# Kernel optimization log

Hardware: AMD Instinct MI355X
Metric: run time of the kernel (lower is better)

The kernel has to match this reference:

```python
import jax, jax.numpy as jnp
import numpy as np

N = 1024          # num_features
H = N // 2        # core dimension (num_params // 2)
NB = 4            # num_blocks
B = 16384         # batch


def _lifted_core(rot_params, diag_params):
    """Build the (N, N) lifted core matrix for one Cayley block."""
    # skew-symmetric matrix from the H rotation params
    S = rot_params[:, None] - rot_params[None, :]            # (H, H)
    I = jnp.eye(H, dtype=rot_params.dtype)
    rotation = jnp.linalg.solve(I - S, I + S)                # Cayley transform
    core = diag_params[:, None] * rotation                   # diag(d) @ rotation
    # rot90(core, k=o) only depends on o mod 4 -> precompute 4 variants
    rots = jnp.stack([core,
                      jnp.rot90(core, 1),
                      jnp.rot90(core, 2),
                      jnp.rot90(core, 3)])                   # (4, H, H)

    def body(lifted, o):
        blk = jax.lax.dynamic_slice(lifted, (o, o), (H, H)) + rots[o % 4]
        return jax.lax.dynamic_update_slice(lifted, blk, (o, o)), None

    lifted, _ = jax.lax.scan(body, jnp.zeros((N, N), dtype=core.dtype),
                             jnp.arange(H + 1))
    return lifted


def setup_inputs() -> dict:
    key = jax.random.key(0)
    ks = jax.random.split(key, 5)
    x = jax.random.normal(ks[0], (B, N), dtype=jnp.float32)
    enc_rot = jax.random.normal(ks[1], (NB, H), dtype=jnp.float32)
    enc_diag = jax.random.normal(ks[2], (NB, H), dtype=jnp.float32)
    dec_rot = jax.random.normal(ks[3], (NB, H), dtype=jnp.float32)
    dec_diag = jax.random.normal(ks[4], (NB, H), dtype=jnp.float32)
    return {"x": x, "enc_rot": enc_rot, "enc_diag": enc_diag,
            "dec_rot": dec_rot, "dec_diag": dec_diag}


def reference(x, enc_rot, enc_diag, dec_rot, dec_diag):
    s = x
    for i in range(NB):                                      # encoder blocks
        s = s @ _lifted_core(enc_rot[i], enc_diag[i]).T
    bottleneck = s
    out = s
    for i in range(NB):                                      # decoder blocks
        out = out @ _lifted_core(dec_rot[i], dec_diag[i]).T
    return bottleneck, out
```

## Files before the change

### kernel.cpp

```cpp
#include <hip/hip_runtime.h>
#include <hip/hip_bf16.h>
#include <cstdint>
#include <cstddef>

#define H 512
#define NFEAT 1024
#define BATCH 16384
#define LM ((size_t)1 << 20)
#define KOP 576

using bf16 = __hip_bfloat16;
using bf16x8 = __attribute__((ext_vector_type(8))) __bf16;
using f32x4 = __attribute__((ext_vector_type(4))) float;
using f32x16 = __attribute__((ext_vector_type(16))) float;

__device__ __forceinline__ void gload16(void* lds, const void* g) {
  __builtin_amdgcn_global_load_lds(
      (__attribute__((address_space(1))) void*)g,
      (__attribute__((address_space(3))) void*)lds,
      16, 0, 0);
}

__global__ void prep_kernel(const float* __restrict__ er, const float* __restrict__ ed,
                            const float* __restrict__ dr, const float* __restrict__ dd,
                            float* __restrict__ ab) {
  const int mat = blockIdx.x;
  const int lane = threadIdx.x;
  const float* u = (mat < 4) ? (er + mat * H) : (dr + (mat - 4) * H);
  const float* d = (mat < 4) ? (ed + mat * H) : (dd + (mat - 4) * H);

  double s = 0.0, q = 0.0;
  for (int k = 0; k < 8; ++k) {
    double v = (double)u[lane + 64 * k];
    s += v;
    q += v * v;
  }
  for (int off = 32; off; off >>= 1) {
    s += __shfl_down(s, off);
    q += __shfl_down(q, off);
  }
  s = __shfl(s, 0);
  q = __shfl(q, 0);

  const double det = 1.0 - s * s + (double)H * q;
  const double cuv = 2.0 * (1.0 + s) / det;
  const double cuu = -2.0 * (double)H / det;
  const double cvv = -2.0 * q / det;
  const double cvu = -2.0 * (1.0 - s) / det;

  float* a = ab + mat * 1024;
  float* b = a + H;
  for (int k = 0; k < 8; ++k) {
    int idx = lane + 64 * k;
    double ui = (double)u[idx], di = (double)d[idx];
    a[idx] = (float)(di * (cuv * ui + cvv));
    b[idx] = (float)(di * (cuu * ui + cvu));
  }
}

__global__ __launch_bounds__(256) void prep2_kernel(
    const float* __restrict__ er, const float* __restrict__ ed,
    const float* __restrict__ dr, const float* __restrict__ dd,
    const float* __restrict__ ab, float* __restrict__ Tpref) {
  __shared__ float buf[4][512];
  __shared__ float tmp[4][512];
  const int mat = blockIdx.x;
  const float* d = (mat < 4) ? (ed + mat * H) : (dd + (mat - 4) * H);
  const float* a = ab + mat * 1024;
  const int t = threadIdx.x;
  for (int m = t; m < 512; m += 256) {
    buf[0][m] = a[m];
    buf[1][m] = a[511 - m];
    buf[2][m] = d[m];
    buf[3][m] = d[511 - m];
  }
  __syncthreads();
  for (int s = 4; s <= 256; s <<= 1) {
    for (int m = t; m < 512; m += 256)
#pragma unroll
      for (int q = 0; q < 4; ++q) tmp[q][m] = (m >= s) ? buf[q][m - s] : 0.f;
    __syncthreads();
    for (int m = t; m < 512; m += 256)
#pragma unroll
      for (int q = 0; q < 4; ++q) buf[q][m] += tmp[q][m];
    __syncthreads();
  }
  float* tp = Tpref + mat * 2048;
  for (int m = t; m < 512; m += 256) {
    tp[m] = buf[0][m];
    tp[512 + m] = buf[1][m];
    tp[1024 + m] = buf[2][m];
    tp[1536 + m] = buf[3][m];
  }
}

__global__ __launch_bounds__(256) void genops_kernel(
    const float* __restrict__ er, const float* __restrict__ dr,
    const float* __restrict__ ab,
    bf16* __restrict__ Ah, bf16* __restrict__ Al,
    bf16* __restrict__ Bh, bf16* __restrict__ Bl) {
  const int x = blockIdx.x;
  const int mat = blockIdx.y;
  const float* u = (mat < 4) ? (er + mat * H) : (dr + (mat - 4) * H);
  const float* b = ab + mat * 1024 + H;
  const int t = threadIdx.x;
  const size_t base = ((size_t)mat * 1024 + x) * KOP;
  for (int k = t; k < KOP; k += 256) {
    float av = 0.f, bv = 0.f;
    if (k <= 128) {
      const int o = 4 * k;
      const int ia = x - o;
      av = (ia >= 0 && ia < 512) ? b[ia] : 0.f;
      bv = (ia >= 0 && ia < 512) ? u[ia] : 0.f;
    } else if (k <= 256) {
      const int o = 4 * (k - 129) + 1;
      const int ia = 511 - x + o;
      const int ib = x - o;
      av = (ia >= 0 && ia < 512) ? u[ia] : 0.f;
      bv = (ib >= 0 && ib < 512) ? b[ib] : 0.f;
    } else if (k <= 384) {
      const int o = 4 * (k - 257) + 2;
      const int ia = 511 - x + o;
      av = (ia >= 0 && ia < 512) ? b[ia] : 0.f;
      bv = (ia >= 0 && ia < 512) ? u[ia] : 0.f;
    } else if (k <= 512) {
      const int o = 4 * (k - 385) + 3;
      const int ia = x - o;
      const int ib = 511 - x + o;
      av = (ia >= 0 && ia < 512) ? u[ia] : 0.f;
      bv = (ib >= 0 && ib < 512) ? b[ib] : 0.f;
    }
    const bf16 ah = __float2bfloat16(av);
    Ah[base + k] = ah;
    Al[base + k] = __float2bfloat16(av - __bfloat162float(ah));
    const bf16 bh = __float2bfloat16(bv);
    Bh[base + k] = bh;
    Bl[base + k] = __float2bfloat16(bv - __bfloat162float(bh));
  }
}

__global__ __launch_bounds__(256) void buildgemm_kernel(
    const bf16* __restrict__ Ah, const bf16* __restrict__ Al,
    const bf16* __restrict__ Bh, const bf16* __restrict__ Bl,
    const float* __restrict__ ed, const float* __restrict__ dd,
    const float* __restrict__ Tpref, bf16* __restrict__ Lbase) {
  __shared__ __align__(16) bf16 smem[4 * 8192];
  __shared__ float pa[512], parev[512], pd[512], pdrev[512], sdl[512];
  bf16* sAh = smem;
  bf16* sAl = smem + 8192;
  bf16* sBh = smem + 16384;
  bf16* sBl = smem + 24576;

  const int tid = threadIdx.x;
  const int lane = tid & 63;
  const int wave = tid >> 6;
  const int wr = wave >> 1;
  const int wc = wave & 1;
  const int mat = blockIdx.z;
  const int row0 = blockIdx.x * 128;
  const int col0 = blockIdx.y * 128;

  {
    const float* tp = Tpref + mat * 2048;
    const float* d = (mat < 4) ? (ed + mat * H) : (dd + (mat - 4) * H);
    for (int m = tid; m < 512; m += 256) {
      pa[m] = tp[m];
      parev[m] = tp[512 + m];
      pd[m] = tp[1024 + m];
      pdrev[m] = tp[1536 + m];
      sdl[m] = d[m];
    }
  }

  const size_t OPS = (size_t)mat * 1024 * KOP;
  const int srow = tid >> 3;
  const int sce = (((tid * 16) ^ (((tid >> 3) & 7) << 4)) & 127) >> 1;
  const size_t abase = OPS + (size_t)(row0 + srow) * KOP + sce;
  const size_t bbase = OPS + (size_t)(col0 + srow) * KOP + sce;
  const int dst0 = tid * 8;

  f32x16 acc[2][2] = {};

  for (int kt = 0; kt < 9; ++kt) {
    const int k0 = kt * 64;
#pragma unroll
    for (int q = 0; q < 4; ++q) {
      const size_t ga = abase + (size_t)(32 * q) * KOP + k0;
      const size_t gb = bbase + (size_t)(32 * q) * KOP + k0;
      const int dq = q * 2048 + dst0;
      gload16(sAh + dq, Ah + ga);
      gload16(sAl + dq, Al + ga);
      gload16(sBh + dq, Bh + gb);
      gload16(sBl + dq, Bl + gb);
    }
    __syncthreads();

    const int l31 = lane & 31;
    const int kh16 = (lane >> 5) * 16;
#pragma unroll
    for (int ks = 0; ks < 4; ++ks) {
      bf16x8 fah[2], fal[2], fbh[2], fbl[2];
#pragma unroll
      for (int m = 0; m < 2; ++m) {
        const int arow = wr * 64 + m * 32 + l31;
        const int abk = (arow * 128 + ks * 32 + kh16) ^ ((arow & 7) << 4);
        fah[m] = *(const bf16x8*)((const char*)sAh + abk);
        fal[m] = *(const bf16x8*)((const char*)sAl + abk);
        const int brow = wc * 64 + m * 32 + l31;
        const int bbk = (brow * 128 + ks * 32 + kh16) ^ ((brow & 7) << 4);
        fbh[m] = *(const bf16x8*)((const char*)sBh + bbk);
        fbl[m] = *(const bf16x8*)((const char*)sBl + bbk);
      }
#pragma unroll
      for (int m = 0; m < 2; ++m)
#pragma unroll
        for (int n = 0; n < 2; ++n) {
          acc[m][n] = __builtin_amdgcn_mfma_f32_32x32x16_bf16(fah[m], fbh[n], acc[m][n], 0, 0, 0);
          acc[m][n] = __builtin_amdgcn_mfma_f32_32x32x16_bf16(fah[m], fbl[n], acc[m][n], 0, 0, 0);
          acc[m][n] = __builtin_amdgcn_mfma_f32_32x32x16_bf16(fal[m], fbh[n], acc[m][n], 0, 0, 0);
        }
    }
    __syncthreads();
  }

  auto apart = [&](int i, int j) -> float {
    const int lo = max(0, max(i, j) - 511);
    const int hi = min(512, min(i, j));
    if (lo > hi) return 0.f;
    float v = 0.f;
    {
      int o1 = lo + ((0 - lo) & 3), o2 = hi - (hi & 3);
      if (o1 <= o2) { int mx = i - o1, mn = i - o2; v += pa[mx] - (mn >= 4 ? pa[mn - 4] : 0.f); }
    }
    {
      int o1 = lo + ((1 - lo) & 3), o2 = hi - ((hi - 1) & 3);
      if (o1 <= o2) { int mx = j - o1, mn = j - o2; v += pa[mx] - (mn >= 4 ? pa[mn - 4] : 0.f); }
    }
    {
      int o1 = lo + ((2 - lo) & 3), o2 = hi - ((hi - 2) & 3);
      if (o1 <= o2) { int mx = i - o1, mn = i - o2; v += parev[mx] - (mn >= 4 ? parev[mn - 4] : 0.f); }
    }
    {
      int o1 = lo + ((3 - lo) & 3), o2 = hi - ((hi - 3) & 3);
      if (o1 <= o2) { int mx = j - o1, mn = j - o2; v += parev[mx] - (mn >= 4 ? parev[mn - 4] : 0.f); }
    }
    if (i == j) {
      {
        int o1 = lo + ((0 - lo) & 3), o2 = hi - (hi & 3);
        if (o1 <= o2) { int mx = i - o1, mn = i - o2; v += pd[mx] - (mn >= 4 ? pd[mn - 4] : 0.f); }
      }
      {
        int o1 = lo + ((2 - lo) & 3), o2 = hi - ((hi - 2) & 3);
        if (o1 <= o2) { int mx = i - o1, mn = i - o2; v += pdrev[mx] - (mn >= 4 ? pdrev[mn - 4] : 0.f); }
      }
    }
    const int m2 = i + j - 511;
    if (m2 >= 0 && !(m2 & 1)) {
      const int os = m2 >> 1;
      if (os >= lo && os <= hi) {
        const int r = os & 3;
        if (r == 1) v += sdl[j - os];
        else if (r == 3) v += sdl[511 - (j - os)];
      }
    }
    return v;
  };

  const int ocol0 = col0 + wc * 64 + (lane & 31);
  const int rb = (lane >> 5) << 2;
#pragma unroll
  for (int m = 0; m < 2; ++m)
#pragma unroll
    for (int n = 0; n < 2; ++n)
#pragma unroll
      for (int r = 0; r < 16; ++r) {
        const int grow = row0 + wr * 64 + m * 32 + (r & 3) + ((r >> 2) << 3) + rb;
        const int gcol = ocol0 + n * 32;
        const float v = acc[m][n][r] + apart(grow, gcol);
        const size_t off = ((size_t)mat << 21) + ((size_t)grow << 10) + (size_t)gcol;
        const bf16 hb = __float2bfloat16(v);
        Lbase[off] = hb;
        Lbase[off + LM] = __float2bfloat16(v - __bfloat162float(hb));
      }
}

__global__ void splith_kernel(const float* __restrict__ x, bf16* __restrict__ h) {
  const int n4 = BATCH * NFEAT / 4;
  int idx = blockIdx.x * blockDim.x + threadIdx.x;
  int stride = gridDim.x * blockDim.x;
  for (int i = idx; i < n4; i += stride) {
    float4 v = ((const float4*)x)[i];
    union { bf16 b[4]; short4 s; } Hu;
    Hu.b[0] = __float2bfloat16(v.x);
    Hu.b[1] = __float2bfloat16(v.y);
    Hu.b[2] = __float2bfloat16(v.z);
    Hu.b[3] = __float2bfloat16(v.w);
    ((short4*)h)[i] = Hu.s;
  }
}

struct TPtrs { const bf16* s; bf16* d; };
struct T6 { TPtrs t[6]; };

__global__ __launch_bounds__(256) void transposeB_kernel(T6 p) {
  const bf16* S = p.t[blockIdx.z].s;
  bf16* D = p.t[blockIdx.z].d;
  __shared__ ushort tile[64][68];
  const int i0 = blockIdx.x * 64, j0 = blockIdx.y * 64;
  const int tid = threadIdx.x;
  const int rr = tid >> 4;
  const int cc = (tid & 15) * 4;
#pragma unroll
  for (int it = 0; it < 4; ++it) {
    const int row = it * 16 + rr;
    const size_t so = (size_t)(i0 + row) * 1024 + j0 + cc;
    ushort4 v = *(const ushort4*)((const ushort*)S + so);
    tile[row][cc] = v.x; tile[row][cc + 1] = v.y;
    tile[row][cc + 2] = v.z; tile[row][cc + 3] = v.w;
  }
  __syncthreads();
#pragma unroll
  for (int it = 0; it < 4; ++it) {
    const int row = it * 16 + rr;
    ushort4 o;
    o.x = tile[cc][row];     o.y = tile[cc + 1][row];
    o.z = tile[cc + 2][row]; o.w = tile[cc + 3][row];
    const size_t dofs = (size_t)(j0 + row) * 1024 + i0 + cc;
    *(ushort4*)((ushort*)D + dofs) = o;
  }
}

struct GPtrs { const bf16* a; const bf16* b; bf16* yh; bf16* yl; };
struct G4 { GPtrs g[4]; };

__global__ __launch_bounds__(256) void chaingemm4_kernel(G4 p) {
  GPtrs q = p.g[blockIdx.z];
  const bf16* A = q.a;
  const bf16* Bh = q.b;
  const bf16* Bl = q.b + LM;

  __shared__ __align__(16) bf16 smem[2 * 3 * 4096];

  const int tid = threadIdx.x;
  const int lane = tid & 63;
  const int wave = tid >> 6;
  const int wr = wave >> 1, wc = wave & 1;
  const int r0 = blockIdx.x * 64, c0 = blockIdx.y * 64;

  const int srow = tid >> 3;
  const int scol = (((tid & 7) ^ (srow & 7))) * 8;
  const int dst = tid * 8;
  const size_t ga0 = (size_t)(r0 + srow) * 1024 + scol;
  const size_t gb0 = (size_t)(c0 + srow) * 1024 + scol;

  auto STAGE = [&](int nb, int k0) {
    bf16* base = smem + nb * 12288;
    gload16(base + dst,        A + ga0 + k0);
    gload16(base + 2048 + dst, A + ga0 + 32 * 1024 + k0);
    gload16(base + 4096 + dst,        Bh + gb0 + k0);
    gload16(base + 4096 + 2048 + dst, Bh + gb0 + 32 * 1024 + k0);
    gload16(base + 8192 + dst,        Bl + gb0 + k0);
    gload16(base + 8192 + 2048 + dst, Bl + gb0 + 32 * 1024 + k0);
  };

  const int l31 = lane & 31;
  const int klg = lane >> 5;
  const int ar = wr * 32 + l31;
  const int br = wc * 32 + l31;
  int aoff[4], boff[4];
#pragma unroll
  for (int ks = 0; ks < 4; ++ks) {
    const int lgA = (ks << 1) | klg;
    aoff[ks] = ar * 64 + ((lgA ^ (ar & 7)) << 3);
    boff[ks] = br * 64 + ((lgA ^ (br & 7)) << 3);
  }

  f32x16 acc = {};

  STAGE(0, 0);
  asm volatile("s_waitcnt vmcnt(0)" ::: "memory");
  __builtin_amdgcn_s_barrier();

  for (int t = 0; t < 16; ++t) {
    const int buf = t & 1;
    const int nb = buf ^ 1;
    const bool pf = (t < 15);
    if (pf) STAGE(nb, (t + 1) * 64);

    const bf16* pA = smem + buf * 12288;
    const bf16* pBh = pA + 4096;
    const bf16* pBl = pA + 8192;
#pragma unroll
    for (int ks = 0; ks < 4; ++ks) {
      bf16x8 ah = *(const bf16x8*)(pA + aoff[ks]);
      bf16x8 bh = *(const bf16x8*)(pBh + boff[ks]);
      bf16x8 bl = *(const bf16x8*)(pBl + boff[ks]);
      acc = __builtin_amdgcn_mfma_f32_32x32x16_bf16(ah, bh, acc, 0, 0, 0);
      acc = __builtin_amdgcn_mfma_f32_32x32x16_bf16(ah, bl, acc, 0, 0, 0);
    }
    if (pf) asm volatile("s_waitcnt vmcnt(0)" ::: "memory");
    __builtin_amdgcn_s_barrier();
  }

  const int oc = c0 + wc * 32 + l31;
  const int rb = (lane >> 5) << 2;
#pragma unroll
  for (int r = 0; r < 16; ++r) {
    const int gr = r0 + wr * 32 + (r & 3) + ((r >> 2) << 3) + rb;
    const size_t off = (size_t)gr * 1024 + oc;
    const float v = acc[r];
    const bf16 hb = __float2bfloat16(v);
    q.yh[off] = hb;
    q.yl[off] = __float2bfloat16(v - __bfloat162float(hb));
  }
}

__global__ __launch_bounds__(512, 1) void gemmbig_kernel(
    const bf16* __restrict__ A, const bf16* __restrict__ Bh_,
    float* __restrict__ Y0, float* __restrict__ Y1) {
  __shared__ __align__(16) bf16 smem[4 * 16384];

  const int tid = threadIdx.x;
  const int lane = tid & 63;
  const int wave = tid >> 6;
  const int wr = wave >> 2;
  const int wc = wave & 3;

  const int pdisp = blockIdx.x + (blockIdx.y << 6);
  const int xcd = pdisp & 7;
  const int chk = pdisp >> 3;
  const int row0 = (xcd * 8 + (chk >> 3)) * 256;
  const int col0 = (chk & 7) * 256;

  const int sr = tid >> 2;
  const int sc = ((tid & 3) ^ ((tid >> 3) & 3)) * 8;
  const size_t abase0 = (size_t)(row0 + sr) * NFEAT + sc;
  const size_t abase1 = (size_t)(row0 + sr + 128) * NFEAT + sc;
  const size_t bbase0 = (size_t)(col0 + sr) * NFEAT + sc;
  const size_t bbase1 = (size_t)(col0 + sr + 128) * NFEAT + sc;
  const int dst = tid * 8;

  auto STAGE_A = [&](int buf, int k0) {
    bf16* base = smem + buf * 16384;
    gload16(base + dst, A + abase0 + k0);
    gload16(base + 4096 + dst, A + abase1 + k0);
  };
  auto STAGE_B = [&](int buf, int k0) {
    bf16* base = smem + buf * 16384 + 8192;
    gload16(base + dst, Bh_ + bbase0 + k0);
    gload16(base + 4096 + dst, Bh_ + bbase1 + k0);
  };

  const int l15 = lane & 15;
  const int kg16 = (lane >> 4) * 16;
  const int swz = ((l15 >> 1) & 3) << 4;
  const int kcol = kg16 ^ swz;
  int aoff[8], boff[4];
#pragma unroll
  for (int fr = 0; fr < 8; ++fr)
    aoff[fr] = (wr * 128 + fr * 16 + l15) * 64 + kcol;
#pragma unroll
  for (int fc = 0; fc < 4; ++fc)
    boff[fc] = (wc * 64 + fc * 16 + l15) * 64 + kcol + 16384;

  auto LD = [&](int buf, int off) {
    return *(const bf16x8*)((const char*)(smem + buf * 16384) + off);
  };

  f32x4 acc[8][4] = {};

  STAGE_A(0, 0); STAGE_B(0, 0);
  STAGE_A(1, 32); STAGE_B(1, 32);
  STAGE_A(2, 64); STAGE_B(2, 64);
  asm volatile("s_waitcnt vmcnt(8)" ::: "memory");
  __builtin_amdgcn_s_barrier();

  for (int T = 0; T < 32; ++T) {
    const int buf = T & 3;
    const int kpre = (T + 3) * 32;
    const bool pf = (T < 29);

    bf16x8 fa[4], fb[4];

    if (pf) STAGE_A((T + 3) & 3, kpre);
#pragma unroll
    for (int fc = 0; fc < 4; ++fc) fb[fc] = LD(buf, boff[fc]);
#pragma unroll
    for (int fr = 0; fr < 4; ++fr) fa[fr] = LD(buf, aoff[fr]);
    __builtin_amdgcn_s_barrier();
    __builtin_amdgcn_s_setprio(1);
#pragma unroll
    for (int fr = 0; fr < 4; ++fr)
#pragma unroll
      for (int fc = 0; fc < 4; ++fc)
        acc[fr][fc] = __builtin_amdgcn_mfma_f32_16x16x32_bf16(fa[fr], fb[fc], acc[fr][fc], 0, 0, 0);
    __builtin_amdgcn_s_setprio(0);
    __builtin_amdgcn_s_barrier();

    if (pf) STAGE_B((T + 3) & 3, kpre);
#pragma unroll
    for (int fr = 0; fr < 4; ++fr) fa[fr] = LD(buf, aoff[4 + fr]);
    __builtin_amdgcn_s_barrier();
    __builtin_amdgcn_s_setprio(1);
#pragma unroll
    for (int fr = 0; fr < 4; ++fr)
#pragma unroll
      for (int fc = 0; fc < 4; ++fc)
        acc[4 + fr][fc] = __builtin_amdgcn_mfma_f32_16x16x32_bf16(fa[fr], fb[fc], acc[4 + fr][fc], 0, 0, 0);
    __builtin_amdgcn_s_setprio(0);
    if (T <= 28) {
      asm volatile("s_waitcnt vmcnt(8)" ::: "memory");
    } else if (T == 29) {
      asm volatile("s_waitcnt vmcnt(4)" ::: "memory");
    } else if (T == 30) {
      asm volatile("s_waitcnt vmcnt(0)" ::: "memory");
    }
    __builtin_amdgcn_s_barrier();
  }

  float* Yb = (col0 < 1024) ? Y0 : (Y1 - 1024);
  const int orow = row0 + wr * 128 + (lane >> 4) * 4;
  const int ocol = col0 + wc * 64 + l15;
#pragma unroll
  for (int fr = 0; fr < 8; ++fr)
#pragma unroll
    for (int fc = 0; fc < 4; ++fc)
#pragma unroll
      for (int r = 0; r < 4; ++r) {
        const int grow = orow + fr * 16 + r;
        const int gcol = ocol + fc * 16;
        Yb[(size_t)grow * NFEAT + (size_t)gcol] = acc[fr][fc][r];
      }
}

extern "C" void kernel_launch(void* const* d_in, const int* in_sizes, int n_in,
                              void* d_out, int out_size, void* d_ws, size_t ws_size,
                              hipStream_t stream) {
  (void)in_sizes; (void)n_in; (void)out_size; (void)ws_size;
  const float* x  = (const float*)d_in[0];
  const float* er = (const float*)d_in[1];
  const float* ed = (const float*)d_in[2];
  const float* dr = (const float*)d_in[3];
  const float* dd = (const float*)d_in[4];

  float* O0 = (float*)d_out;
  float* O1 = O0 + (size_t)BATCH * NFEAT;

  bf16* Lb = (bf16*)d_ws;
  float* ab = (float*)(Lb + 16 * LM);
  bf16* Qh = (bf16*)(ab + 8 * 1024);

  float* Tpref = O0;
  bf16* SB = (bf16*)((char*)O0 + (1 << 20));
  auto slot = [&](int s) { return SB + (size_t)s * LM; };

  const size_t OPN = (size_t)8 * 1024 * KOP;
  bf16* Aoph = (bf16*)O1;
  bf16* Aopl = Aoph + OPN;
  bf16* Boph = Aopl + OPN;
  bf16* Bopl = Boph + OPN;

  prep_kernel<<<8, 64, 0, stream>>>(er, ed, dr, dd, ab);
  prep2_kernel<<<8, 256, 0, stream>>>(er, ed, dr, dd, ab, Tpref);
  genops_kernel<<<dim3(1024, 8), 256, 0, stream>>>(er, dr, ab, Aoph, Aopl, Boph, Bopl);
  buildgemm_kernel<<<dim3(8, 8, 8), 256, 0, stream>>>(Aoph, Aopl, Boph, Bopl,
                                                      ed, dd, Tpref, Lb);
  splith_kernel<<<4096, 256, 0, stream>>>(x, Qh);

  {
    T6 p;
    p.t[0] = {Lb + 0 * LM,  slot(0)};
    p.t[1] = {Lb + 4 * LM,  slot(2)};
    p.t[2] = {Lb + 5 * LM,  slot(3)};
    p.t[3] = {Lb + 8 * LM,  slot(4)};
    p.t[4] = {Lb + 12 * LM, slot(6)};
    p.t[5] = {Lb + 13 * LM, slot(7)};
    transposeB_kernel<<<dim3(16, 16, 6), 256, 0, stream>>>(p);
  }
  {
    G4 p;
    p.g[0] = {slot(0),      Lb + 2 * LM,  slot(8),  slot(9)};
    p.g[1] = {Lb + 6 * LM,  slot(2),      slot(10), slot(11)};
    p.g[2] = {slot(4),      Lb + 10 * LM, slot(12), slot(13)};
    p.g[3] = {Lb + 14 * LM, slot(6),      slot(14), slot(15)};
    chaingemm4_kernel<<<dim3(16, 16, 4), 256, 0, stream>>>(p);
  }
  {
    G4 p;
    p.g[0] = {slot(8),  slot(10), slot(0), slot(1)};
    p.g[1] = {slot(12), slot(14), slot(2), slot(3)};
    p.g[2] = p.g[0];
    p.g[3] = p.g[1];
    chaingemm4_kernel<<<dim3(16, 16, 2), 256, 0, stream>>>(p);
  }
  {
    T6 p;
    p.t[0] = {slot(0), Lb + 0 * LM};
    p.t[1] = {slot(2), Lb + 2 * LM};
    p.t[2] = p.t[0]; p.t[3] = p.t[0]; p.t[4] = p.t[0]; p.t[5] = p.t[0];
    transposeB_kernel<<<dim3(16, 16, 2), 256, 0, stream>>>(p);
  }
  {
    G4 p;
    p.g[0] = {Lb + 2 * LM, slot(0), Lb + 1 * LM, slot(4)};
    p.g[1] = p.g[0]; p.g[2] = p.g[0]; p.g[3] = p.g[0];
    chaingemm4_kernel<<<dim3(16, 16, 1), 256, 0, stream>>>(p);
  }

  gemmbig_kernel<<<dim3(64, 8), 512, 0, stream>>>(Qh, Lb, O0, O1);
}
```

Measured before the change: 257.2 us.

## Retile big GEMM to 128x256 tiles with 256 threads, two blocks per CU

The final large GEMM moves from 256x256 tiles on 512-thread blocks (one per CU) with a 4-deep LDS ring to 128x256 tiles on 256-thread blocks with a 3-deep ring, so two blocks can share a CU. The intra-iteration barriers between the A and B staging halves are removed, and each wave now owns a 64x128 output sub-tile. The aim is more overlap between blocks and less synchronisation overhead. In exchange, arithmetic intensity per tile drops, prefetch depth is shorter, and the grid grows to 1024 blocks.

```diff
diff --git a/kernel.cpp b/kernel.cpp
--- a/kernel.cpp
+++ b/kernel.cpp
@@ -415,79 +415,76 @@
   }
 }
 
-__global__ __launch_bounds__(512, 1) void gemmbig_kernel(
+__global__ __launch_bounds__(256, 2) void gemmbig_kernel(
     const bf16* __restrict__ A, const bf16* __restrict__ Bh_,
     float* __restrict__ Y0, float* __restrict__ Y1) {
-  __shared__ __align__(16) bf16 smem[4 * 16384];
+  __shared__ __align__(16) bf16 smem[3 * 12288];
 
   const int tid = threadIdx.x;
   const int lane = tid & 63;
   const int wave = tid >> 6;
-  const int wr = wave >> 2;
-  const int wc = wave & 3;
-
-  const int pdisp = blockIdx.x + (blockIdx.y << 6);
+  const int wr = wave >> 1;
+  const int wc = wave & 1;
+
+  const int pdisp = blockIdx.x;
   const int xcd = pdisp & 7;
   const int chk = pdisp >> 3;
-  const int row0 = (xcd * 8 + (chk >> 3)) * 256;
+  const int row0 = (xcd * 16 + (chk >> 3)) * 128;
   const int col0 = (chk & 7) * 256;
 
   const int sr = tid >> 2;
   const int sc = ((tid & 3) ^ ((tid >> 3) & 3)) * 8;
   const size_t abase0 = (size_t)(row0 + sr) * NFEAT + sc;
-  const size_t abase1 = (size_t)(row0 + sr + 128) * NFEAT + sc;
-  const size_t bbase0 = (size_t)(col0 + sr) * NFEAT + sc;
-  const size_t bbase1 = (size_t)(col0 + sr + 128) * NFEAT + sc;
+  const size_t abase1 = abase0 + (size_t)64 * NFEAT;
+  const size_t bbase = (size_t)(col0 + sr) * NFEAT + sc;
   const int dst = tid * 8;
 
   auto STAGE_A = [&](int buf, int k0) {
-    bf16* base = smem + buf * 16384;
+    bf16* base = smem + buf * 12288;
     gload16(base + dst, A + abase0 + k0);
-    gload16(base + 4096 + dst, A + abase1 + k0);
+    gload16(base + 2048 + dst, A + abase1 + k0);
   };
   auto STAGE_B = [&](int buf, int k0) {
-    bf16* base = smem + buf * 16384 + 8192;
-    gload16(base + dst, Bh_ + bbase0 + k0);
-    gload16(base + 4096 + dst, Bh_ + bbase1 + k0);
+    bf16* base = smem + buf * 12288 + 4096;
+#pragma unroll
+    for (int q = 0; q < 4; ++q)
+      gload16(base + q * 2048 + dst, Bh_ + bbase + (size_t)(64 * q) * NFEAT + k0);
   };
 
   const int l15 = lane & 15;
-  const int kg16 = (lane >> 4) * 16;
-  const int swz = ((l15 >> 1) & 3) << 4;
-  const int kcol = kg16 ^ swz;
-  int aoff[8], boff[4];
-#pragma unroll
-  for (int fr = 0; fr < 8; ++fr)
-    aoff[fr] = (wr * 128 + fr * 16 + l15) * 64 + kcol;
-#pragma unroll
-  for (int fc = 0; fc < 4; ++fc)
-    boff[fc] = (wc * 64 + fc * 16 + l15) * 64 + kcol + 16384;
+  const int kcol = ((lane >> 4) * 16) ^ (((l15 >> 1) & 3) << 4);
+  int aoff[4], boff[8];
+#pragma unroll
+  for (int fr = 0; fr < 4; ++fr)
+    aoff[fr] = (wr * 64 + fr * 16 + l15) * 64 + kcol;
+#pragma unroll
+  for (int fc = 0; fc < 8; ++fc)
+    boff[fc] = 8192 + (wc * 128 + fc * 16 + l15) * 64 + kcol;
 
   auto LD = [&](int buf, int off) {
-    return *(const bf16x8*)((const char*)(smem + buf * 16384) + off);
+    return *(const bf16x8*)((const char*)(smem + buf * 12288) + off);
   };
 
-  f32x4 acc[8][4] = {};
+  f32x4 acc[4][8] = {};
 
   STAGE_A(0, 0); STAGE_B(0, 0);
   STAGE_A(1, 32); STAGE_B(1, 32);
-  STAGE_A(2, 64); STAGE_B(2, 64);
-  asm volatile("s_waitcnt vmcnt(8)" ::: "memory");
+  asm volatile("s_waitcnt vmcnt(6)" ::: "memory");
   __builtin_amdgcn_s_barrier();
 
   for (int T = 0; T < 32; ++T) {
-    const int buf = T & 3;
-    const int kpre = (T + 3) * 32;
-    const bool pf = (T < 29);
+    const int buf = T % 3;
+    if (T < 30) {
+      const int nb = (T + 2) % 3;
+      STAGE_A(nb, (T + 2) * 32);
+      STAGE_B(nb, (T + 2) * 32);
+    }
 
     bf16x8 fa[4], fb[4];
-
-    if (pf) STAGE_A((T + 3) & 3, kpre);
+#pragma unroll
+    for (int fr = 0; fr < 4; ++fr) fa[fr] = LD(buf, aoff[fr]);
 #pragma unroll
     for (int fc = 0; fc < 4; ++fc) fb[fc] = LD(buf, boff[fc]);
-#pragma unroll
-    for (int fr = 0; fr < 4; ++fr) fa[fr] = LD(buf, aoff[fr]);
-    __builtin_amdgcn_s_barrier();
     __builtin_amdgcn_s_setprio(1);
 #pragma unroll
     for (int fr = 0; fr < 4; ++fr)
@@ -495,23 +492,18 @@
       for (int fc = 0; fc < 4; ++fc)
         acc[fr][fc] = __builtin_amdgcn_mfma_f32_16x16x32_bf16(fa[fr], fb[fc], acc[fr][fc], 0, 0, 0);
     __builtin_amdgcn_s_setprio(0);
-    __builtin_amdgcn_s_barrier();
-
-    if (pf) STAGE_B((T + 3) & 3, kpre);
-#pragma unroll
-    for (int fr = 0; fr < 4; ++fr) fa[fr] = LD(buf, aoff[4 + fr]);
-    __builtin_amdgcn_s_barrier();
+#pragma unroll
+    for (int fc = 0; fc < 4; ++fc) fb[fc] = LD(buf, boff[4 + fc]);
     __builtin_amdgcn_s_setprio(1);
 #pragma unroll
     for (int fr = 0; fr < 4; ++fr)
 #pragma unroll
       for (int fc = 0; fc < 4; ++fc)
-        acc[4 + fr][fc] = __builtin_amdgcn_mfma_f32_16x16x32_bf16(fa[fr], fb[fc], acc[4 + fr][fc], 0, 0, 0);
+        acc[fr][4 + fc] = __builtin_amdgcn_mfma_f32_16x16x32_bf16(fa[fr], fb[fc], acc[fr][4 + fc], 0, 0, 0);
     __builtin_amdgcn_s_setprio(0);
-    if (T <= 28) {
-      asm volatile("s_waitcnt vmcnt(8)" ::: "memory");
-    } else if (T == 29) {
-      asm volatile("s_waitcnt vmcnt(4)" ::: "memory");
+
+    if (T <= 29) {
+      asm volatile("s_waitcnt vmcnt(6)" ::: "memory");
     } else if (T == 30) {
       asm volatile("s_waitcnt vmcnt(0)" ::: "memory");
     }
@@ -519,12 +511,12 @@
   }
 
   float* Yb = (col0 < 1024) ? Y0 : (Y1 - 1024);
-  const int orow = row0 + wr * 128 + (lane >> 4) * 4;
-  const int ocol = col0 + wc * 64 + l15;
-#pragma unroll
-  for (int fr = 0; fr < 8; ++fr)
-#pragma unroll
-    for (int fc = 0; fc < 4; ++fc)
+  const int orow = row0 + wr * 64 + (lane >> 4) * 4;
+  const int ocol = col0 + wc * 128 + l15;
+#pragma unroll
+  for (int fr = 0; fr < 4; ++fr)
+#pragma unroll
+    for (int fc = 0; fc < 8; ++fc)
 #pragma unroll
       for (int r = 0; r < 4; ++r) {
         const int grow = orow + fr * 16 + r;
@@ -607,5 +599,5 @@
     chaingemm4_kernel<<<dim3(16, 16, 1), 256, 0, stream>>>(p);
   }
 
-  gemmbig_kernel<<<dim3(64, 8), 512, 0, stream>>>(Qh, Lb, O0, O1);
-}
+  gemmbig_kernel<<<1024, 256, 0, stream>>>(Qh, Lb, O0, O1);
+}
```

New measurement: 253.1 us. Within noise of the previous version (-1.6%).
